# Optimization experiments

Hardware: AMD Instinct MI355X
Metric: run time of the kernel (lower is better)

The kernel has to match this reference:

```python
import jax, jax.numpy as jnp
import numpy as np

BT, N, C, H, W = 1, 4, 64, 28, 60
ZC, YC, XC = 200, 8, 200  # grid dims (Zcam, Ycam, Xcam); voxel_shape=[200,200,8] -> Z=200, X=200, Y=8
OUT_C = 128
EPS = 1e-6


def setup_inputs() -> dict:
    key = jax.random.key(0)
    k1, k2, k3, k4 = jax.random.split(key, 4)
    # normalized sampling coords in ~[-1.2, 1.2] so some points fall outside the image (zero-padded)
    voxcam_coords = jax.random.uniform(k1, (BT, N, ZC, YC, XC, 3), jnp.float32, -1.2, 1.2)
    # binary visibility mask per voxel-camera pair
    vox_valid = (jax.random.uniform(k2, (BT, N, ZC, YC, XC, 1)) < 0.5).astype(jnp.float32)
    img_feats = jax.random.normal(k3, (BT, N, C, H, W), jnp.float32)
    W_comp = jax.random.normal(k4, (OUT_C, C * YC), jnp.float32) * 0.02  # MLP-as-1x1-conv height compressor
    b_comp = jnp.zeros((OUT_C,), jnp.float32)
    return {"voxcam_coords": voxcam_coords, "vox_valid": vox_valid, "img_feats": img_feats,
            "W_comp": W_comp, "b_comp": b_comp}


def _grid_sample_3d(feat, grid):
    """Trilinear grid_sample, align_corners=False, zeros padding.
    feat: (B, C, D, H, W); grid: (B, P, 3) with (x, y, z) in [-1, 1]. Returns (B, C, P)."""
    B, Cc, D, Hh, Ww = feat.shape
    x = ((grid[..., 0] + 1.0) * Ww - 1.0) * 0.5
    y = ((grid[..., 1] + 1.0) * Hh - 1.0) * 0.5
    z = ((grid[..., 2] + 1.0) * D - 1.0) * 0.5
    x0f, y0f, z0f = jnp.floor(x), jnp.floor(y), jnp.floor(z)
    wx, wy, wz = x - x0f, y - y0f, z - z0f
    x0, y0, z0 = x0f.astype(jnp.int32), y0f.astype(jnp.int32), z0f.astype(jnp.int32)

    def sample_one(fb, x0b, y0b, z0b, wxb, wyb, wzb):
        out = jnp.zeros((Cc, x0b.shape[0]), fb.dtype)
        for dz in (0, 1):
            for dy in (0, 1):
                for dx in (0, 1):
                    zi, yi, xi = z0b + dz, y0b + dy, x0b + dx
                    valid = ((zi >= 0) & (zi < D) & (yi >= 0) & (yi < Hh)
                             & (xi >= 0) & (xi < Ww)).astype(fb.dtype)
                    v = fb[:, jnp.clip(zi, 0, D - 1), jnp.clip(yi, 0, Hh - 1), jnp.clip(xi, 0, Ww - 1)]
                    w = ((wxb if dx else 1.0 - wxb) * (wyb if dy else 1.0 - wyb)
                         * (wzb if dz else 1.0 - wzb)) * valid
                    out = out + v * w[None]
        return out

    return jax.vmap(sample_one)(feat, x0, y0, z0, wx, wy, wz)


def reference(voxcam_coords, vox_valid, img_feats, W_comp, b_comp):
    bt, n, zc, yc, xc, _ = voxcam_coords.shape
    c, h, w = img_feats.shape[2], img_feats.shape[3], img_feats.shape[4]
    P = zc * yc * xc
    grid = voxcam_coords.reshape(bt * n, P, 3)
    feat = img_feats.reshape(bt * n, c, 1, h, w)  # N_group=1 depth axis
    sampled = _grid_sample_3d(feat, grid).reshape(bt, n, c, zc, yc, xc)
    mask = jnp.transpose(vox_valid, (0, 1, 5, 2, 3, 4))  # (bt, n, 1, zc, yc, xc)
    vox_feats = sampled * mask                      # get_feats_dense_grid_sample masking
    # reduce_cams: masked mean over cameras (dim=1)
    red = (vox_feats * mask).sum(axis=1) / (mask.sum(axis=1) + EPS)  # (bt, c, zc, yc, xc)
    # height compressor: 'bt c z y x -> bt (c y) z x' then 1x1 conv (MLP)
    comp_in = jnp.transpose(red, (0, 1, 3, 2, 4)).reshape(bt, c * yc, zc, xc)
    out = jnp.einsum('bczx,oc->bozx', comp_in, W_comp) + b_comp[None, :, None, None]
    # _unpack_batch: (b*t, C, Z, X) -> (b, t, C, Z, X) with b=t=1
    return out.reshape(1, bt, out.shape[1], zc, xc)
```

## Files before the change

kernel.cpp:

```cpp
#include <hip/hip_runtime.h>
#include <hip/hip_bf16.h>
#include <hip/hip_fp16.h>

#define N_  4
#define C_  64
#define H_  28
#define W_  60
#define ZC_ 200
#define YC_ 8
#define XC_ 200
#define OUTC_ 128
#define KD_ 512
#define EPS_ 1e-6f
#define ZB 4
#define XB 8
#define NCOL 32

typedef __attribute__((ext_vector_type(8))) _Float16 half8;
typedef __attribute__((ext_vector_type(4))) float f32x4;
typedef __attribute__((ext_vector_type(4))) unsigned int u32x4;

__global__ void gsvt_prep(const float* __restrict__ img,
                          const float* __restrict__ Wc,
                          __half* __restrict__ featH,
                          __half* __restrict__ WbH) {
    int tid = blockIdx.x * blockDim.x + threadIdx.x;
    int stride = gridDim.x * blockDim.x;
    const int totF = N_ * H_ * W_ * C_;
    for (int i = tid; i < totF; i += stride) {
        int c  = i & 63;
        int hw = i >> 6;
        int w  = hw % W_;
        int nh = hw / W_;
        int h  = nh % H_;
        int n  = nh / H_;
        featH[i] = __float2half(img[((n * C_ + c) * H_ + h) * W_ + w]);
    }
    const int totW = OUTC_ * KD_;
    for (int i = tid; i < totW; i += stride) {
        int k = i & (KD_ - 1);
        int o = i >> 9;
        int y = k >> 6;
        int c = k & 63;
        WbH[i] = __float2half(Wc[o * KD_ + c * YC_ + y]);
    }
}

__device__ __forceinline__ void accq(__half2* n, const u32x4 V, const unsigned wp) {
    const __half2 w2 = *(const __half2*)&wp;
    unsigned vx = V.x, vy = V.y, vz = V.z, vw = V.w;
    n[0] = __hfma2(w2, *(const __half2*)&vx, n[0]);
    n[1] = __hfma2(w2, *(const __half2*)&vy, n[1]);
    n[2] = __hfma2(w2, *(const __half2*)&vz, n[2]);
    n[3] = __hfma2(w2, *(const __half2*)&vw, n[3]);
}

__global__ __launch_bounds__(256, 3) void gsvt_fusedF(
        const float* __restrict__ coords,
        const float* __restrict__ validm,
        const __half* __restrict__ featH,
        const __half* __restrict__ WbH,
        const float* __restrict__ bias,
        float* __restrict__ out)
{
    __shared__ uint4 tab[N_ * 256];
    __shared__ unsigned short redB[64][NCOL][8];
    float (*ms)[4] = (float(*)[4])&redB[0][0][0];

    const int z0 = blockIdx.y * ZB;
    const int x0 = blockIdx.x * XB;
    const int t  = threadIdx.x;

    const int p0   = t;
    const int y0_  = t >> 5;
    const int col0 = t & 31;
    const int zg   = z0 + (col0 >> 3);
    const int xg   = x0 + (col0 & 7);

    float gx[4], gy[4], gzv[4], mm[4];
    #pragma unroll
    for (int cam = 0; cam < N_; ++cam) {
        const int cb = ((cam * ZC_ + zg) * YC_ + y0_) * XC_ + xg;
        gx[cam]  = coords[cb * 3 + 0];
        gy[cam]  = coords[cb * 3 + 1];
        gzv[cam] = coords[cb * 3 + 2];
        mm[cam]  = validm[cb];
        ms[p0][cam] = mm[cam];
    }
    __syncthreads();

    {
        const float inv = 1.0f / (ms[p0][0] + ms[p0][1] + ms[p0][2] + ms[p0][3] + EPS_);
        #pragma unroll
        for (int cam = 0; cam < N_; ++cam) {
            const float xf = ((gx[cam] + 1.0f) * (float)W_ - 1.0f) * 0.5f;
            const float yf = ((gy[cam] + 1.0f) * (float)H_ - 1.0f) * 0.5f;
            const float zf = gzv[cam] * 0.5f;
            const float x0f = floorf(xf), y0f = floorf(yf), z0f = floorf(zf);
            const float wx = xf - x0f, wy = yf - y0f, wz = zf - z0f;
            const int xi = (int)x0f, yi = (int)y0f, zi = (int)z0f;

            const float zw = (zi == 0) ? (1.f - wz) : ((zi == -1) ? wz : 0.f);
            const float s  = mm[cam] * zw * inv;

            const float wx0 = (xi >= 0 && xi < W_)         ? (1.f - wx) * s : 0.f;
            const float wx1 = (xi + 1 >= 0 && xi + 1 < W_) ? wx * s         : 0.f;
            const float wy0 = (yi >= 0 && yi < H_)         ? (1.f - wy)     : 0.f;
            const float wy1 = (yi + 1 >= 0 && yi + 1 < H_) ? wy             : 0.f;

            const unsigned h00 = __half_as_ushort(__float2half(wy0 * wx0));
            const unsigned h01 = __half_as_ushort(__float2half(wy0 * wx1));
            const unsigned h10 = __half_as_ushort(__float2half(wy1 * wx0));
            const unsigned h11 = __half_as_ushort(__float2half(wy1 * wx1));

            const int xc0 = min(max(xi, 0), W_ - 1);
            const int xc1 = min(max(xi + 1, 0), W_ - 1);
            const int yc0 = min(max(yi, 0), H_ - 1);
            const int yc1 = min(max(yi + 1, 0), H_ - 1);
            const unsigned base = (unsigned)((((cam * H_ + yc0) * W_) + xc0) * 128);
            const unsigned dxo  = (unsigned)((xc1 - xc0) * 128);
            const unsigned dyo  = (unsigned)((yc1 - yc0) * W_ * 128);
            tab[cam * 256 + p0] = make_uint4(h00 | (h01 << 16), h10 | (h11 << 16),
                                             base, dxo | (dyo << 16));
        }
    }
    __syncthreads();

    const int grp   = t >> 3;
    const int lane8 = t & 7;
    const unsigned lb = (unsigned)(lane8 << 4);
    const char* fb = (const char*)featH;

    #define ISSUE(V, A_) asm volatile("global_load_dwordx4 %0, %1, off" \
                                      : "=v"(V) : "v"(A_))
    #define WAITV(n) do { asm volatile("s_waitcnt vmcnt(" #n ")"); \
                          __builtin_amdgcn_sched_barrier(0); } while (0)

    #pragma unroll
    for (int y = 0; y < YC_; ++y) {
        const int p = y * 32 + grp;

        const uint4 T0 = tab[0 * 256 + p];
        const uint4 T1 = tab[1 * 256 + p];
        const uint4 T2 = tab[2 * 256 + p];
        const uint4 T3 = tab[3 * 256 + p];

        u32x4 V00, V01, V02, V03, V10, V11, V12, V13;
        u32x4 V20, V21, V22, V23, V30, V31, V32, V33;
        #define ADDR_ISSUE(Tv, Va, Vb, Vc, Vd)                                 \
            {                                                                  \
                const bool act = (Tv.x | Tv.y) != 0u;                          \
                const unsigned base = act ? (Tv.z + lb) : lb;                  \
                const unsigned dxo  = act ? (Tv.w & 0xFFFFu) : 0u;             \
                const unsigned dyo  = act ? (Tv.w >> 16) : 0u;                 \
                ISSUE(Va, fb + base);                                          \
                ISSUE(Vb, fb + (base + dxo));                                  \
                ISSUE(Vc, fb + (base + dyo));                                  \
                ISSUE(Vd, fb + (base + dyo + dxo));                            \
            }
        ADDR_ISSUE(T0, V00, V01, V02, V03)
        ADDR_ISSUE(T1, V10, V11, V12, V13)
        ADDR_ISSUE(T2, V20, V21, V22, V23)
        ADDR_ISSUE(T3, V30, V31, V32, V33)
        #undef ADDR_ISSUE

        __half2 zz2 = __half2half2(__ushort_as_half(0));
        __half2 num[4] = {zz2, zz2, zz2, zz2};

        #define BLO(u) (((u) & 0xFFFFu) | ((u) << 16))
        #define BHI(u) (((u) & 0xFFFF0000u) | ((u) >> 16))

        WAITV(12);
        accq(num, V00, BLO(T0.x)); accq(num, V01, BHI(T0.x));
        accq(num, V02, BLO(T0.y)); accq(num, V03, BHI(T0.y));
        WAITV(8);
        accq(num, V10, BLO(T1.x)); accq(num, V11, BHI(T1.x));
        accq(num, V12, BLO(T1.y)); accq(num, V13, BHI(T1.y));
        WAITV(4);
        accq(num, V20, BLO(T2.x)); accq(num, V21, BHI(T2.x));
        accq(num, V22, BLO(T2.y)); accq(num, V23, BHI(T2.y));
        WAITV(0);
        accq(num, V30, BLO(T3.x)); accq(num, V31, BHI(T3.x));
        accq(num, V32, BLO(T3.y)); accq(num, V33, BHI(T3.y));
        #undef BLO
        #undef BHI

        const int kb   = y * 8 + lane8;
        const int pcol = (grp & 16) | ((grp ^ kb) & 15);
        *(uint4*)&redB[kb][pcol][0] =
            make_uint4(*(unsigned*)&num[0], *(unsigned*)&num[1],
                       *(unsigned*)&num[2], *(unsigned*)&num[3]);
    }
    #undef ISSUE
    #undef WAITV
    __syncthreads();

    const int wave = t >> 6;
    const int lane = t & 63;
    const int q    = lane >> 4;
    const int l16  = lane & 15;

    f32x4 acc00 = {0.f,0.f,0.f,0.f}, acc01 = {0.f,0.f,0.f,0.f};
    f32x4 acc10 = {0.f,0.f,0.f,0.f}, acc11 = {0.f,0.f,0.f,0.f};
    const __half* wbase = WbH + (wave * 32 + l16) * KD_;

    #pragma unroll
    for (int ks = 0; ks < 16; ++ks) {
        const int kb = ks * 4 + q;
        const int xs = l16 ^ (kb & 15);
        const half8 B0 = *(const half8*)&redB[kb][xs][0];
        const half8 B1 = *(const half8*)&redB[kb][16 + xs][0];
        const half8 A0 = *(const half8*)(wbase + ks * 32 + q * 8);
        const half8 A1 = *(const half8*)(wbase + 16 * KD_ + ks * 32 + q * 8);
        acc00 = __builtin_amdgcn_mfma_f32_16x16x32_f16(A0, B0, acc00, 0, 0, 0);
        acc01 = __builtin_amdgcn_mfma_f32_16x16x32_f16(A0, B1, acc01, 0, 0, 0);
        acc10 = __builtin_amdgcn_mfma_f32_16x16x32_f16(A1, B0, acc10, 0, 0, 0);
        acc11 = __builtin_amdgcn_mfma_f32_16x16x32_f16(A1, B1, acc11, 0, 0, 0);
    }

    #pragma unroll
    for (int ct = 0; ct < 2; ++ct) {
        const int c2  = ct * 16 + l16;
        const int zz  = c2 >> 3;
        const int xl  = c2 & 7;
        const int ob  = (z0 + zz) * XC_ + x0 + xl;
        const f32x4 a0 = ct ? acc01 : acc00;
        const f32x4 a1 = ct ? acc11 : acc10;
        #pragma unroll
        for (int j = 0; j < 4; ++j) {
            const int o0 = wave * 32 + q * 4 + j;
            out[o0 * (ZC_ * XC_) + ob] = a0[j] + bias[o0];
            const int o1 = o0 + 16;
            out[o1 * (ZC_ * XC_) + ob] = a1[j] + bias[o1];
        }
    }
}

extern "C" void kernel_launch(void* const* d_in, const int* in_sizes, int n_in,
                              void* d_out, int out_size, void* d_ws, size_t ws_size,
                              hipStream_t stream) {
    const float* coords = (const float*)d_in[0];
    const float* validm = (const float*)d_in[1];
    const float* img    = (const float*)d_in[2];
    const float* Wc     = (const float*)d_in[3];
    const float* bias   = (const float*)d_in[4];
    float* out = (float*)d_out;

    __half* featH = (__half*)d_ws;
    __half* WbH   = featH + (N_ * H_ * W_ * C_);

    gsvt_prep<<<512, 256, 0, stream>>>(img, Wc, featH, WbH);

    dim3 grid(XC_ / XB, ZC_ / ZB);
    gsvt_fusedF<<<grid, 256, 0, stream>>>(coords, validm, featH, WbH, bias, out);
}
```

Before: 54.98 us.

## Software-pipeline gather loads across height slices with split camera batches

Restructures the per-y gather loop into a two-stage software pipeline. The next slice's loads for cameras 0-1 are issued before waiting on cameras 2-3 of the current slice, and the waits are tied to specific registers so the compiler cannot reorder around them. The goal is to hide global-load latency across iterations instead of draining all loads every slice. This raises register pressure, so launch bounds drop from 3 to 2 blocks per CU, which lowers occupancy.

```diff
diff --git a/kernel.cpp b/kernel.cpp
--- a/kernel.cpp
+++ b/kernel.cpp
@@ -55,7 +55,17 @@
     n[3] = __hfma2(w2, *(const __half2*)&vw, n[3]);
 }
 
-__global__ __launch_bounds__(256, 3) void gsvt_fusedF(
+__device__ __forceinline__ void mkaddr(const uint4 T, const unsigned lb,
+                                       unsigned& a0, unsigned& a1,
+                                       unsigned& a2, unsigned& a3) {
+    const bool act = (T.x | T.y) != 0u;
+    const unsigned base = act ? (T.z + lb) : lb;
+    const unsigned dxo  = act ? (T.w & 0xFFFFu) : 0u;
+    const unsigned dyo  = act ? (T.w >> 16) : 0u;
+    a0 = base; a1 = base + dxo; a2 = base + dyo; a3 = base + dyo + dxo;
+}
+
+__global__ __launch_bounds__(256, 2) void gsvt_fusedP(
         const float* __restrict__ coords,
         const float* __restrict__ validm,
         const __half* __restrict__ featH,
@@ -133,66 +143,91 @@
 
     #define ISSUE(V, A_) asm volatile("global_load_dwordx4 %0, %1, off" \
                                       : "=v"(V) : "v"(A_))
-    #define WAITV(n) do { asm volatile("s_waitcnt vmcnt(" #n ")"); \
-                          __builtin_amdgcn_sched_barrier(0); } while (0)
-
-    #pragma unroll
-    for (int y = 0; y < YC_; ++y) {
-        const int p = y * 32 + grp;
-
-        const uint4 T0 = tab[0 * 256 + p];
-        const uint4 T1 = tab[1 * 256 + p];
-        const uint4 T2 = tab[2 * 256 + p];
-        const uint4 T3 = tab[3 * 256 + p];
-
-        u32x4 V00, V01, V02, V03, V10, V11, V12, V13;
-        u32x4 V20, V21, V22, V23, V30, V31, V32, V33;
-        #define ADDR_ISSUE(Tv, Va, Vb, Vc, Vd)                                 \
-            {                                                                  \
-                const bool act = (Tv.x | Tv.y) != 0u;                          \
-                const unsigned base = act ? (Tv.z + lb) : lb;                  \
-                const unsigned dxo  = act ? (Tv.w & 0xFFFFu) : 0u;             \
-                const unsigned dyo  = act ? (Tv.w >> 16) : 0u;                 \
-                ISSUE(Va, fb + base);                                          \
-                ISSUE(Vb, fb + (base + dxo));                                  \
-                ISSUE(Vc, fb + (base + dyo));                                  \
-                ISSUE(Vd, fb + (base + dyo + dxo));                            \
-            }
-        ADDR_ISSUE(T0, V00, V01, V02, V03)
-        ADDR_ISSUE(T1, V10, V11, V12, V13)
-        ADDR_ISSUE(T2, V20, V21, V22, V23)
-        ADDR_ISSUE(T3, V30, V31, V32, V33)
-        #undef ADDR_ISSUE
-
-        __half2 zz2 = __half2half2(__ushort_as_half(0));
-        __half2 num[4] = {zz2, zz2, zz2, zz2};
-
-        #define BLO(u) (((u) & 0xFFFFu) | ((u) << 16))
-        #define BHI(u) (((u) & 0xFFFF0000u) | ((u) >> 16))
-
-        WAITV(12);
-        accq(num, V00, BLO(T0.x)); accq(num, V01, BHI(T0.x));
-        accq(num, V02, BLO(T0.y)); accq(num, V03, BHI(T0.y));
-        WAITV(8);
-        accq(num, V10, BLO(T1.x)); accq(num, V11, BHI(T1.x));
-        accq(num, V12, BLO(T1.y)); accq(num, V13, BHI(T1.y));
-        WAITV(4);
-        accq(num, V20, BLO(T2.x)); accq(num, V21, BHI(T2.x));
-        accq(num, V22, BLO(T2.y)); accq(num, V23, BHI(T2.y));
-        WAITV(0);
-        accq(num, V30, BLO(T3.x)); accq(num, V31, BHI(T3.x));
-        accq(num, V32, BLO(T3.y)); accq(num, V33, BHI(T3.y));
-        #undef BLO
-        #undef BHI
-
-        const int kb   = y * 8 + lane8;
-        const int pcol = (grp & 16) | ((grp ^ kb) & 15);
-        *(uint4*)&redB[kb][pcol][0] =
-            make_uint4(*(unsigned*)&num[0], *(unsigned*)&num[1],
-                       *(unsigned*)&num[2], *(unsigned*)&num[3]);
-    }
+    #define WAIT8_8(a,b,c,d,e,f,g,h)                                        \
+        asm volatile("s_waitcnt vmcnt(8)"                                    \
+            : "+v"(a), "+v"(b), "+v"(c), "+v"(d),                            \
+              "+v"(e), "+v"(f), "+v"(g), "+v"(h))
+    #define WAIT8_0(a,b,c,d,e,f,g,h)                                        \
+        asm volatile("s_waitcnt vmcnt(0)"                                    \
+            : "+v"(a), "+v"(b), "+v"(c), "+v"(d),                            \
+              "+v"(e), "+v"(f), "+v"(g), "+v"(h))
+
+    #define BLO(u) (((u) & 0xFFFFu) | ((u) << 16))
+    #define BHI(u) (((u) & 0xFFFF0000u) | ((u) >> 16))
+
+    u32x4 A0v, A1v, A2v, A3v, B0v, B1v, B2v, B3v;
+    u32x4 C0v, C1v, C2v, C3v, D0v, D1v, D2v, D3v;
+    uint4 T0, T1, T2, T3;
+
+    {
+        T0 = tab[0 * 256 + grp];
+        T1 = tab[1 * 256 + grp];
+        T2 = tab[2 * 256 + grp];
+        T3 = tab[3 * 256 + grp];
+        unsigned a0,a1,a2,a3, b0,b1,b2,b3;
+        mkaddr(T0, lb, a0,a1,a2,a3);
+        mkaddr(T1, lb, b0,b1,b2,b3);
+        ISSUE(A0v, fb + a0); ISSUE(A1v, fb + a1);
+        ISSUE(A2v, fb + a2); ISSUE(A3v, fb + a3);
+        ISSUE(B0v, fb + b0); ISSUE(B1v, fb + b1);
+        ISSUE(B2v, fb + b2); ISSUE(B3v, fb + b3);
+    }
+
+    #define SBODY(Y, ISNEXT)                                                 \
+    {                                                                        \
+                                               \
+        unsigned a0,a1,a2,a3, b0,b1,b2,b3;                                   \
+        mkaddr(T2, lb, a0,a1,a2,a3);                                         \
+        mkaddr(T3, lb, b0,b1,b2,b3);                                         \
+        ISSUE(C0v, fb + a0); ISSUE(C1v, fb + a1);                            \
+        ISSUE(C2v, fb + a2); ISSUE(C3v, fb + a3);                            \
+        ISSUE(D0v, fb + b0); ISSUE(D1v, fb + b1);                            \
+        ISSUE(D2v, fb + b2); ISSUE(D3v, fb + b3);                            \
+                           \
+        WAIT8_8(A0v,A1v,A2v,A3v, B0v,B1v,B2v,B3v);                           \
+        __half2 z2 = __half2half2(__ushort_as_half(0));                      \
+        __half2 num[4] = {z2, z2, z2, z2};                                   \
+        accq(num, A0v, BLO(T0.x)); accq(num, A1v, BHI(T0.x));                \
+        accq(num, A2v, BLO(T0.y)); accq(num, A3v, BHI(T0.y));                \
+        accq(num, B0v, BLO(T1.x)); accq(num, B1v, BHI(T1.x));                \
+        accq(num, B2v, BLO(T1.y)); accq(num, B3v, BHI(T1.y));                \
+        const uint4 S2 = T2, S3 = T3;                                        \
+        if (ISNEXT) {                                                        \
+                        \
+            const int pn = ((Y) + 1) * 32 + grp;                             \
+            T0 = tab[0 * 256 + pn]; T1 = tab[1 * 256 + pn];                  \
+            T2 = tab[2 * 256 + pn]; T3 = tab[3 * 256 + pn];                  \
+            unsigned c0,c1,c2,c3, d0,d1,d2,d3;                               \
+            mkaddr(T0, lb, c0,c1,c2,c3);                                     \
+            mkaddr(T1, lb, d0,d1,d2,d3);                                     \
+            ISSUE(A0v, fb + c0); ISSUE(A1v, fb + c1);                        \
+            ISSUE(A2v, fb + c2); ISSUE(A3v, fb + c3);                        \
+            ISSUE(B0v, fb + d0); ISSUE(B1v, fb + d1);                        \
+            ISSUE(B2v, fb + d2); ISSUE(B3v, fb + d3);                        \
+            WAIT8_8(C0v,C1v,C2v,C3v, D0v,D1v,D2v,D3v);                       \
+        } else {                                                             \
+            WAIT8_0(C0v,C1v,C2v,C3v, D0v,D1v,D2v,D3v);                       \
+        }                                                                    \
+        accq(num, C0v, BLO(S2.x)); accq(num, C1v, BHI(S2.x));                \
+        accq(num, C2v, BLO(S2.y)); accq(num, C3v, BHI(S2.y));                \
+        accq(num, D0v, BLO(S3.x)); accq(num, D1v, BHI(S3.x));                \
+        accq(num, D2v, BLO(S3.y)); accq(num, D3v, BHI(S3.y));                \
+        const int kb   = (Y) * 8 + lane8;                                    \
+        const int pcol = (grp & 16) | ((grp ^ kb) & 15);                     \
+        unsigned n0 = *(unsigned*)&num[0], n1 = *(unsigned*)&num[1];         \
+        unsigned n2 = *(unsigned*)&num[2], n3 = *(unsigned*)&num[3];         \
+        *(uint4*)&redB[kb][pcol][0] = make_uint4(n0, n1, n2, n3);            \
+    }
+
+    SBODY(0, 1) SBODY(1, 1) SBODY(2, 1) SBODY(3, 1)
+    SBODY(4, 1) SBODY(5, 1) SBODY(6, 1) SBODY(7, 0)
+
+    #undef SBODY
     #undef ISSUE
-    #undef WAITV
+    #undef WAIT8_8
+    #undef WAIT8_0
+    #undef BLO
+    #undef BHI
     __syncthreads();
 
     const int wave = t >> 6;
@@ -208,14 +243,14 @@
     for (int ks = 0; ks < 16; ++ks) {
         const int kb = ks * 4 + q;
         const int xs = l16 ^ (kb & 15);
-        const half8 B0 = *(const half8*)&redB[kb][xs][0];
-        const half8 B1 = *(const half8*)&redB[kb][16 + xs][0];
-        const half8 A0 = *(const half8*)(wbase + ks * 32 + q * 8);
-        const half8 A1 = *(const half8*)(wbase + 16 * KD_ + ks * 32 + q * 8);
-        acc00 = __builtin_amdgcn_mfma_f32_16x16x32_f16(A0, B0, acc00, 0, 0, 0);
-        acc01 = __builtin_amdgcn_mfma_f32_16x16x32_f16(A0, B1, acc01, 0, 0, 0);
-        acc10 = __builtin_amdgcn_mfma_f32_16x16x32_f16(A1, B0, acc10, 0, 0, 0);
-        acc11 = __builtin_amdgcn_mfma_f32_16x16x32_f16(A1, B1, acc11, 0, 0, 0);
+        const half8 Bf0 = *(const half8*)&redB[kb][xs][0];
+        const half8 Bf1 = *(const half8*)&redB[kb][16 + xs][0];
+        const half8 Af0 = *(const half8*)(wbase + ks * 32 + q * 8);
+        const half8 Af1 = *(const half8*)(wbase + 16 * KD_ + ks * 32 + q * 8);
+        acc00 = __builtin_amdgcn_mfma_f32_16x16x32_f16(Af0, Bf0, acc00, 0, 0, 0);
+        acc01 = __builtin_amdgcn_mfma_f32_16x16x32_f16(Af0, Bf1, acc01, 0, 0, 0);
+        acc10 = __builtin_amdgcn_mfma_f32_16x16x32_f16(Af1, Bf0, acc10, 0, 0, 0);
+        acc11 = __builtin_amdgcn_mfma_f32_16x16x32_f16(Af1, Bf1, acc11, 0, 0, 0);
     }
 
     #pragma unroll
@@ -252,5 +287,5 @@
     gsvt_prep<<<512, 256, 0, stream>>>(img, Wc, featH, WbH);
 
     dim3 grid(XC_ / XB, ZC_ / ZB);
-    gsvt_fusedF<<<grid, 256, 0, stream>>>(coords, validm, featH, WbH, bias, out);
-}
+    gsvt_fusedP<<<grid, 256, 0, stream>>>(coords, validm, featH, WbH, bias, out);
+}
```

Result: no change. 55.39 us (+0.7%).

## Halve block tile to 16 columns and split camera/height work across threads

Applied to the files above, without the earlier changes.

Shrinks each block's output tile from 4x8 to 2x8 (z,x) columns, doubling the grid. The 256 threads now cover the coefficient table by splitting camera pairs, and the gather loop by splitting height slices, rather than each thread handling all cameras or all heights. Shared memory use drops and launch bounds rise to 5 blocks per CU to improve occupancy and latency hiding. In exchange the MFMA stage reuses each weight fragment across only one column tile, and global weight loads per output double.

```diff
diff --git a/kernel.cpp b/kernel.cpp
--- a/kernel.cpp
+++ b/kernel.cpp
@@ -12,9 +12,9 @@
 #define OUTC_ 128
 #define KD_ 512
 #define EPS_ 1e-6f
-#define ZB 4
+#define ZB 2
 #define XB 8
-#define NCOL 32
+#define NCOL 16
 
 typedef __attribute__((ext_vector_type(8))) _Float16 half8;
 typedef __attribute__((ext_vector_type(4))) float f32x4;
@@ -55,7 +55,7 @@
     n[3] = __hfma2(w2, *(const __half2*)&vw, n[3]);
 }
 
-__global__ __launch_bounds__(256, 3) void gsvt_fusedF(
+__global__ __launch_bounds__(256, 5) void gsvt_fused16F(
         const float* __restrict__ coords,
         const float* __restrict__ validm,
         const __half* __restrict__ featH,
@@ -63,7 +63,7 @@
         const float* __restrict__ bias,
         float* __restrict__ out)
 {
-    __shared__ uint4 tab[N_ * 256];
+    __shared__ uint4 tab[N_ * 128];
     __shared__ unsigned short redB[64][NCOL][8];
     float (*ms)[4] = (float(*)[4])&redB[0][0][0];
 
@@ -71,37 +71,40 @@
     const int x0 = blockIdx.x * XB;
     const int t  = threadIdx.x;
 
-    const int p0   = t;
-    const int y0_  = t >> 5;
-    const int col0 = t & 31;
+    const int p0   = t & 127;
+    const int y0_  = p0 >> 4;
+    const int col0 = p0 & 15;
     const int zg   = z0 + (col0 >> 3);
     const int xg   = x0 + (col0 & 7);
-
-    float gx[4], gy[4], gzv[4], mm[4];
-    #pragma unroll
-    for (int cam = 0; cam < N_; ++cam) {
+    const int cam0 = (t >> 7) * 2;
+
+    float gx[2], gy[2], gzv[2], mm[2];
+    #pragma unroll
+    for (int ii = 0; ii < 2; ++ii) {
+        const int cam = cam0 + ii;
         const int cb = ((cam * ZC_ + zg) * YC_ + y0_) * XC_ + xg;
-        gx[cam]  = coords[cb * 3 + 0];
-        gy[cam]  = coords[cb * 3 + 1];
-        gzv[cam] = coords[cb * 3 + 2];
-        mm[cam]  = validm[cb];
-        ms[p0][cam] = mm[cam];
+        gx[ii]  = coords[cb * 3 + 0];
+        gy[ii]  = coords[cb * 3 + 1];
+        gzv[ii] = coords[cb * 3 + 2];
+        mm[ii]  = validm[cb];
+        ms[p0][cam] = mm[ii];
     }
     __syncthreads();
 
     {
         const float inv = 1.0f / (ms[p0][0] + ms[p0][1] + ms[p0][2] + ms[p0][3] + EPS_);
         #pragma unroll
-        for (int cam = 0; cam < N_; ++cam) {
-            const float xf = ((gx[cam] + 1.0f) * (float)W_ - 1.0f) * 0.5f;
-            const float yf = ((gy[cam] + 1.0f) * (float)H_ - 1.0f) * 0.5f;
-            const float zf = gzv[cam] * 0.5f;
+        for (int ii = 0; ii < 2; ++ii) {
+            const int cam = cam0 + ii;
+            const float xf = ((gx[ii] + 1.0f) * (float)W_ - 1.0f) * 0.5f;
+            const float yf = ((gy[ii] + 1.0f) * (float)H_ - 1.0f) * 0.5f;
+            const float zf = gzv[ii] * 0.5f;
             const float x0f = floorf(xf), y0f = floorf(yf), z0f = floorf(zf);
             const float wx = xf - x0f, wy = yf - y0f, wz = zf - z0f;
             const int xi = (int)x0f, yi = (int)y0f, zi = (int)z0f;
 
             const float zw = (zi == 0) ? (1.f - wz) : ((zi == -1) ? wz : 0.f);
-            const float s  = mm[cam] * zw * inv;
+            const float s  = mm[ii] * zw * inv;
 
             const float wx0 = (xi >= 0 && xi < W_)         ? (1.f - wx) * s : 0.f;
             const float wx1 = (xi + 1 >= 0 && xi + 1 < W_) ? wx * s         : 0.f;
@@ -120,7 +123,7 @@
             const unsigned base = (unsigned)((((cam * H_ + yc0) * W_) + xc0) * 128);
             const unsigned dxo  = (unsigned)((xc1 - xc0) * 128);
             const unsigned dyo  = (unsigned)((yc1 - yc0) * W_ * 128);
-            tab[cam * 256 + p0] = make_uint4(h00 | (h01 << 16), h10 | (h11 << 16),
+            tab[cam * 128 + p0] = make_uint4(h00 | (h01 << 16), h10 | (h11 << 16),
                                              base, dxo | (dyo << 16));
         }
     }
@@ -128,6 +131,8 @@
 
     const int grp   = t >> 3;
     const int lane8 = t & 7;
+    const int col   = grp & 15;
+    const int ybase = (grp >> 4) * 4;
     const unsigned lb = (unsigned)(lane8 << 4);
     const char* fb = (const char*)featH;
 
@@ -137,13 +142,14 @@
                           __builtin_amdgcn_sched_barrier(0); } while (0)
 
     #pragma unroll
-    for (int y = 0; y < YC_; ++y) {
-        const int p = y * 32 + grp;
-
-        const uint4 T0 = tab[0 * 256 + p];
-        const uint4 T1 = tab[1 * 256 + p];
-        const uint4 T2 = tab[2 * 256 + p];
-        const uint4 T3 = tab[3 * 256 + p];
+    for (int i = 0; i < 4; ++i) {
+        const int y = ybase + i;
+        const int p = y * 16 + col;
+
+        const uint4 T0 = tab[0 * 128 + p];
+        const uint4 T1 = tab[1 * 128 + p];
+        const uint4 T2 = tab[2 * 128 + p];
+        const uint4 T3 = tab[3 * 128 + p];
 
         u32x4 V00, V01, V02, V03, V10, V11, V12, V13;
         u32x4 V20, V21, V22, V23, V30, V31, V32, V33;
@@ -186,10 +192,10 @@
         #undef BHI
 
         const int kb   = y * 8 + lane8;
-        const int pcol = (grp & 16) | ((grp ^ kb) & 15);
-        *(uint4*)&redB[kb][pcol][0] =
-            make_uint4(*(unsigned*)&num[0], *(unsigned*)&num[1],
-                       *(unsigned*)&num[2], *(unsigned*)&num[3]);
+        const int pcol = col ^ (kb & 15);
+        unsigned n0 = *(unsigned*)&num[0], n1 = *(unsigned*)&num[1];
+        unsigned n2 = *(unsigned*)&num[2], n3 = *(unsigned*)&num[3];
+        *(uint4*)&redB[kb][pcol][0] = make_uint4(n0, n1, n2, n3);
     }
     #undef ISSUE
     #undef WAITV
@@ -200,39 +206,27 @@
     const int q    = lane >> 4;
     const int l16  = lane & 15;
 
-    f32x4 acc00 = {0.f,0.f,0.f,0.f}, acc01 = {0.f,0.f,0.f,0.f};
-    f32x4 acc10 = {0.f,0.f,0.f,0.f}, acc11 = {0.f,0.f,0.f,0.f};
+    f32x4 acc0 = {0.f,0.f,0.f,0.f}, acc1 = {0.f,0.f,0.f,0.f};
     const __half* wbase = WbH + (wave * 32 + l16) * KD_;
 
     #pragma unroll
     for (int ks = 0; ks < 16; ++ks) {
         const int kb = ks * 4 + q;
         const int xs = l16 ^ (kb & 15);
-        const half8 B0 = *(const half8*)&redB[kb][xs][0];
-        const half8 B1 = *(const half8*)&redB[kb][16 + xs][0];
+        const half8 Bf = *(const half8*)&redB[kb][xs][0];
         const half8 A0 = *(const half8*)(wbase + ks * 32 + q * 8);
         const half8 A1 = *(const half8*)(wbase + 16 * KD_ + ks * 32 + q * 8);
-        acc00 = __builtin_amdgcn_mfma_f32_16x16x32_f16(A0, B0, acc00, 0, 0, 0);
-        acc01 = __builtin_amdgcn_mfma_f32_16x16x32_f16(A0, B1, acc01, 0, 0, 0);
-        acc10 = __builtin_amdgcn_mfma_f32_16x16x32_f16(A1, B0, acc10, 0, 0, 0);
-        acc11 = __builtin_amdgcn_mfma_f32_16x16x32_f16(A1, B1, acc11, 0, 0, 0);
-    }
-
-    #pragma unroll
-    for (int ct = 0; ct < 2; ++ct) {
-        const int c2  = ct * 16 + l16;
-        const int zz  = c2 >> 3;
-        const int xl  = c2 & 7;
-        const int ob  = (z0 + zz) * XC_ + x0 + xl;
-        const f32x4 a0 = ct ? acc01 : acc00;
-        const f32x4 a1 = ct ? acc11 : acc10;
-        #pragma unroll
-        for (int j = 0; j < 4; ++j) {
-            const int o0 = wave * 32 + q * 4 + j;
-            out[o0 * (ZC_ * XC_) + ob] = a0[j] + bias[o0];
-            const int o1 = o0 + 16;
-            out[o1 * (ZC_ * XC_) + ob] = a1[j] + bias[o1];
-        }
+        acc0 = __builtin_amdgcn_mfma_f32_16x16x32_f16(A0, Bf, acc0, 0, 0, 0);
+        acc1 = __builtin_amdgcn_mfma_f32_16x16x32_f16(A1, Bf, acc1, 0, 0, 0);
+    }
+
+    const int ob = (z0 + (l16 >> 3)) * XC_ + x0 + (l16 & 7);
+    #pragma unroll
+    for (int j = 0; j < 4; ++j) {
+        const int o0 = wave * 32 + q * 4 + j;
+        out[o0 * (ZC_ * XC_) + ob] = acc0[j] + bias[o0];
+        const int o1 = o0 + 16;
+        out[o1 * (ZC_ * XC_) + ob] = acc1[j] + bias[o1];
     }
 }
 
@@ -252,5 +246,5 @@
     gsvt_prep<<<512, 256, 0, stream>>>(img, Wc, featH, WbH);
 
     dim3 grid(XC_ / XB, ZC_ / ZB);
-    gsvt_fusedF<<<grid, 256, 0, stream>>>(coords, validm, featH, WbH, bias, out);
-}
+    gsvt_fused16F<<<grid, 256, 0, stream>>>(coords, validm, featH, WbH, bias, out);
+}
```

After: 70.59 us. 1.28x slower.
